# Performance work log

Measured on AMD Instinct MI355X. Metric: run time of the kernel, lower is better.

Reference implementation:

```python
import jax, jax.numpy as jnp
import numpy as np

N = 1048576
INPUT_CH = 3
INPUT_CH_VIEWS = 3
HIDDEN = 64
GEO_FEAT = 15


def setup_inputs() -> dict:
    key = jax.random.key(0)
    ks = jax.random.split(key, 8)
    def w(k, out_d, in_d):
        # torch nn.Linear default init: U(-1/sqrt(in), 1/sqrt(in)), weight shape [out, in]
        bound = 1.0 / np.sqrt(in_d)
        return jax.random.uniform(k, (out_d, in_d), jnp.float32, -bound, bound)
    return {
        "x": jax.random.normal(ks[0], (N, INPUT_CH + INPUT_CH_VIEWS), jnp.float32),
        "sw0": w(ks[1], HIDDEN, INPUT_CH),
        "sw1": w(ks[2], HIDDEN, HIDDEN),
        "sw2": w(ks[3], 1 + GEO_FEAT, HIDDEN),
        "cw0": w(ks[4], HIDDEN, INPUT_CH_VIEWS + GEO_FEAT),
        "cw1": w(ks[5], HIDDEN, HIDDEN),
        "cw2": w(ks[6], HIDDEN, HIDDEN),
        "cw3": w(ks[7], 3, HIDDEN),
    }


def reference(x, sw0, sw1, sw2, cw0, cw1, cw2, cw3):
    input_pts = x[..., :INPUT_CH]          # [N, 3]
    input_views = x[..., INPUT_CH:]        # [N, 3]

    # sigma network: Linear(no bias) + ReLU (no ReLU on last layer)
    h = jax.nn.relu(input_pts @ sw0.T)     # [N, 64]
    h = jax.nn.relu(h @ sw1.T)             # [N, 64]
    h = h @ sw2.T                          # [N, 16]
    sigma = h[..., 0]                      # [N]
    geo_feat = h[..., 1:]                  # [N, 15]

    # color network
    h = jnp.concatenate([input_views, geo_feat], axis=-1)  # [N, 18]
    h = jax.nn.relu(h @ cw0.T)             # [N, 64]
    h = jax.nn.relu(h @ cw1.T)             # [N, 64]
    h = jax.nn.relu(h @ cw2.T)             # [N, 64]
    color = h @ cw3.T                      # [N, 3]

    return jnp.concatenate([color, sigma[..., None]], axis=-1)  # [N, 4]
```

## Files before the change

### kernel.cpp

```cpp
#include <hip/hip_runtime.h>
#include <stdint.h>

typedef __attribute__((ext_vector_type(8))) _Float16 half8;
typedef __attribute__((ext_vector_type(2))) __fp16 fp16x2;
typedef __attribute__((ext_vector_type(16))) float floatx16;
typedef __attribute__((ext_vector_type(2))) short s16x2;
typedef unsigned int u32;
typedef unsigned short u16;


__device__ __forceinline__ u32 pkf16(float a, float b) {
  union { fp16x2 v; u32 u; } c;
  c.v = __builtin_amdgcn_cvt_pkrtz(a, b);
  return c.u;
}

__device__ __forceinline__ u32 relu_pk(u32 t) {
  union { u32 u; s16x2 v; } c;
  c.u = t;
  s16x2 zz = {0, 0};
  c.v = __builtin_elementwise_max(c.v, zz);
  return c.u;
}

__device__ __forceinline__ u16 rtnh(float a) {
  union { _Float16 h; u16 u; } c;
  c.h = (_Float16)a;
  return c.u;
}

__device__ __forceinline__ int sigperm(int k) {
  int r = k & 15;
  int s = (r & 3) | ((r & 4) << 1) | ((r & 8) >> 1);
  return (k & ~15) | s;
}

__device__ __forceinline__ half8 packhalf(const floatx16 a, int base, bool relu) {
  union { u32 u[4]; half8 v; } r;
#pragma unroll
  for (int i = 0; i < 4; ++i) {
    u32 t = pkf16(a[base + 2 * i], a[base + 2 * i + 1]);
    r.u[i] = relu ? relu_pk(t) : t;
  }
  return r.v;
}

#define MFMA(A, B, C) __builtin_amdgcn_mfma_f32_32x32x16_f16(A, B, C, 0, 0, 0)

#define NFRAG 38

__global__ void build_pool(
    const float* __restrict__ w_s0, const float* __restrict__ w_s1,
    const float* __restrict__ w_s2, const float* __restrict__ w_c0,
    const float* __restrict__ w_c1, const float* __restrict__ w_c2,
    const float* __restrict__ w_c3, uint4* __restrict__ pool) {
  const int f = blockIdx.x;
  const int lane = threadIdx.x;
  const int m = lane & 31;
  const int kb = (lane >> 5) << 3;

  union { u16 e[8]; uint4 q; } u;
  if (f < 2) {
    const int row = f * 32 + m;
#pragma unroll
    for (int j = 0; j < 8; ++j) {
      const int k = kb + j;
      u.e[j] = (k < 3) ? rtnh(w_s0[row * 3 + k]) : (u16)0;
    }
  } else if (f < 10) {
    const int g = f - 2, rt = g >> 2, ks = g & 3;
    const int row = rt * 32 + m;
#pragma unroll
    for (int j = 0; j < 8; ++j)
      u.e[j] = rtnh(w_s1[row * 64 + sigperm(ks * 16 + kb + j)]);
  } else if (f < 14) {
    const int ks = f - 10;
    const int row = (m < 16) ? m : 0;
#pragma unroll
    for (int j = 0; j < 8; ++j) {
      u16 v = rtnh(w_s2[row * 64 + sigperm(ks * 16 + kb + j)]);
      u.e[j] = (m < 16) ? v : (u16)0;
    }
  } else if (f < 18) {
    const int g = f - 14, rt = g >> 1, ks = g & 1;
    const int row = rt * 32 + m;
#pragma unroll
    for (int j = 0; j < 8; ++j) {
      if (ks == 0) {
        const int c = sigperm(kb + j);
        u16 v = rtnh(w_c0[row * 18 + (c + 2)]);
        u.e[j] = (c == 0) ? (u16)0 : v;
      } else {
        const int kk = kb + j;
        u16 v = rtnh(w_c0[row * 18 + kk]);
        u.e[j] = (kk < 3) ? v : (u16)0;
      }
    }
  } else if (f < 26) {
    const int g = f - 18, rt = g >> 2, ks = g & 3;
    const int row = rt * 32 + m;
#pragma unroll
    for (int j = 0; j < 8; ++j)
      u.e[j] = rtnh(w_c1[row * 64 + sigperm(ks * 16 + kb + j)]);
  } else if (f < 34) {
    const int g = f - 26, rt = g >> 2, ks = g & 3;
    const int row = rt * 32 + m;
#pragma unroll
    for (int j = 0; j < 8; ++j)
      u.e[j] = rtnh(w_c2[row * 64 + sigperm(ks * 16 + kb + j)]);
  } else {
    const int ks = f - 34;
    const int row = (m < 3) ? m : 0;
#pragma unroll
    for (int j = 0; j < 8; ++j) {
      u16 v = rtnh(w_c3[row * 64 + sigperm(ks * 16 + kb + j)]);
      u.e[j] = (m < 3) ? v : (u16)0;
    }
  }
  pool[f * 64 + lane] = u.q;
}

__global__ __launch_bounds__(256, 2) void nerf_fused(
    const float* __restrict__ x, const uint4* __restrict__ pool,
    float* __restrict__ out, int npts) {
  __shared__ __align__(16) u16 wl[NFRAG * 512];

  {
    uint4* lp = (uint4*)wl;
    for (int i = threadIdx.x; i < NFRAG * 64; i += 256) lp[i] = pool[i];
  }
  __syncthreads();

  const int lane = threadIdx.x & 63;
  const int wid = threadIdx.x >> 6;
  const int m = lane & 31;
  const int hi = lane >> 5;

#define LD(F) (*(const half8*)(wl + (F) * 512 + lane * 8))
#define U4 _Pragma("unroll") for (int s = 0; s < 4; ++s)

  const int ntiles = npts >> 5;
  const int wgid = blockIdx.x * 4 + wid;
  const int tile0 = wgid * 4;
  if (tile0 + 4 > ntiles) return;

  const floatx16 z = (floatx16)0.0f;

  union bfrag { u32 u[4]; half8 v; };
  bfrag bx[4], bv[4];
  int pt[4];
  U4 {
    pt[s] = ((tile0 + s) << 5) | m;
    const float2* xp = (const float2*)(x + (size_t)pt[s] * 6);
    const float2 a0 = xp[0], a1 = xp[1], a2 = xp[2];
    bx[s].u[0] = hi ? 0u : pkf16(a0.x, a0.y);
    bx[s].u[1] = hi ? 0u : pkf16(a1.x, 0.0f);
    bx[s].u[2] = 0u; bx[s].u[3] = 0u;
    bv[s].u[0] = hi ? 0u : pkf16(a1.y, a2.x);
    bv[s].u[1] = hi ? 0u : pkf16(a2.y, 0.0f);
    bv[s].u[2] = 0u; bv[s].u[3] = 0u;
  }

  floatx16 h0[4], h1[4];
  half8 b0[4], b1[4], b2[4], b3[4];
  half8 w;

  w = LD(0); U4 h0[s] = MFMA(w, bx[s].v, z);
  w = LD(1); U4 h1[s] = MFMA(w, bx[s].v, z);
  U4 { b0[s] = packhalf(h0[s], 0, true); b1[s] = packhalf(h0[s], 8, true);
       b2[s] = packhalf(h1[s], 0, true); b3[s] = packhalf(h1[s], 8, true); }

  w = LD(2); U4 h0[s] = MFMA(w, b0[s], z);
  w = LD(6); U4 h1[s] = MFMA(w, b0[s], z);
  w = LD(3); U4 h0[s] = MFMA(w, b1[s], h0[s]);
  w = LD(7); U4 h1[s] = MFMA(w, b1[s], h1[s]);
  w = LD(4); U4 h0[s] = MFMA(w, b2[s], h0[s]);
  w = LD(8); U4 h1[s] = MFMA(w, b2[s], h1[s]);
  w = LD(5); U4 h0[s] = MFMA(w, b3[s], h0[s]);
  w = LD(9); U4 h1[s] = MFMA(w, b3[s], h1[s]);
  U4 { b0[s] = packhalf(h0[s], 0, true); b1[s] = packhalf(h0[s], 8, true);
       b2[s] = packhalf(h1[s], 0, true); b3[s] = packhalf(h1[s], 8, true); }

  w = LD(10); U4 h0[s] = MFMA(w, b0[s], z);
  w = LD(11); U4 h0[s] = MFMA(w, b1[s], h0[s]);
  w = LD(12); U4 h0[s] = MFMA(w, b2[s], h0[s]);
  w = LD(13); U4 h0[s] = MFMA(w, b3[s], h0[s]);
  float sigma[4];
  half8 bs2[4];
  U4 { sigma[s] = h0[s][0]; bs2[s] = packhalf(h0[s], 0, false); }

  w = LD(14); U4 h0[s] = MFMA(w, bs2[s], z);
  w = LD(16); U4 h1[s] = MFMA(w, bs2[s], z);
  w = LD(15); U4 h0[s] = MFMA(w, bv[s].v, h0[s]);
  w = LD(17); U4 h1[s] = MFMA(w, bv[s].v, h1[s]);
  U4 { b0[s] = packhalf(h0[s], 0, true); b1[s] = packhalf(h0[s], 8, true);
       b2[s] = packhalf(h1[s], 0, true); b3[s] = packhalf(h1[s], 8, true); }

  w = LD(18); U4 h0[s] = MFMA(w, b0[s], z);
  w = LD(22); U4 h1[s] = MFMA(w, b0[s], z);
  w = LD(19); U4 h0[s] = MFMA(w, b1[s], h0[s]);
  w = LD(23); U4 h1[s] = MFMA(w, b1[s], h1[s]);
  w = LD(20); U4 h0[s] = MFMA(w, b2[s], h0[s]);
  w = LD(24); U4 h1[s] = MFMA(w, b2[s], h1[s]);
  w = LD(21); U4 h0[s] = MFMA(w, b3[s], h0[s]);
  w = LD(25); U4 h1[s] = MFMA(w, b3[s], h1[s]);
  U4 { b0[s] = packhalf(h0[s], 0, true); b1[s] = packhalf(h0[s], 8, true);
       b2[s] = packhalf(h1[s], 0, true); b3[s] = packhalf(h1[s], 8, true); }

  w = LD(26); U4 h0[s] = MFMA(w, b0[s], z);
  w = LD(30); U4 h1[s] = MFMA(w, b0[s], z);
  w = LD(27); U4 h0[s] = MFMA(w, b1[s], h0[s]);
  w = LD(31); U4 h1[s] = MFMA(w, b1[s], h1[s]);
  w = LD(28); U4 h0[s] = MFMA(w, b2[s], h0[s]);
  w = LD(32); U4 h1[s] = MFMA(w, b2[s], h1[s]);
  w = LD(29); U4 h0[s] = MFMA(w, b3[s], h0[s]);
  w = LD(33); U4 h1[s] = MFMA(w, b3[s], h1[s]);
  U4 { b0[s] = packhalf(h0[s], 0, true); b1[s] = packhalf(h0[s], 8, true);
       b2[s] = packhalf(h1[s], 0, true); b3[s] = packhalf(h1[s], 8, true); }

  w = LD(34); U4 h0[s] = MFMA(w, b0[s], z);
  w = LD(35); U4 h0[s] = MFMA(w, b1[s], h0[s]);
  w = LD(36); U4 h0[s] = MFMA(w, b2[s], h0[s]);
  w = LD(37); U4 h0[s] = MFMA(w, b3[s], h0[s]);

  if (lane < 32) {
    U4 {
      float4 o;
      o.x = h0[s][0]; o.y = h0[s][1]; o.z = h0[s][2]; o.w = sigma[s];
      *(float4*)(out + (size_t)pt[s] * 4) = o;
    }
  }
#undef LD
#undef U4
}

extern "C" void kernel_launch(void* const* d_in, const int* in_sizes, int n_in,
                              void* d_out, int out_size, void* d_ws, size_t ws_size,
                              hipStream_t stream) {
  const float* x = (const float*)d_in[0];
  const float* sw0 = (const float*)d_in[1];
  const float* sw1 = (const float*)d_in[2];
  const float* sw2 = (const float*)d_in[3];
  const float* cw0 = (const float*)d_in[4];
  const float* cw1 = (const float*)d_in[5];
  const float* cw2 = (const float*)d_in[6];
  const float* cw3 = (const float*)d_in[7];
  float* out = (float*)d_out;
  uint4* pool = (uint4*)d_ws;

  const int npts = in_sizes[0] / 6;
  const int ntiles = npts >> 5;
  const int blocks = (ntiles + 15) / 16;

  build_pool<<<NFRAG, 64, 0, stream>>>(sw0, sw1, sw2, cw0, cw1, cw2, cw3, pool);
  nerf_fused<<<blocks, 256, 0, stream>>>(x, pool, out, npts);
}
```

Measured before the change: 115.3 us.

## Keep weight fragments in registers and loop over tiles per wave

Removes the shared-memory weight staging and barrier. Each wave now loads 34 weight fragments straight from global memory into registers and keeps them for a serial loop over 8 tiles, with the last-layer fragments reloaded every iteration. The grid shrinks to match. This cuts LDS traffic and the per-block pool copy, but each tile now runs a single dependent MFMA chain instead of 4 interleaved ones, so latency hiding and register pressure (about 136 VGPRs of weights) may get worse.

```diff
diff --git a/kernel.cpp b/kernel.cpp
--- a/kernel.cpp
+++ b/kernel.cpp
@@ -7,6 +7,8 @@
 typedef __attribute__((ext_vector_type(2))) short s16x2;
 typedef unsigned int u32;
 typedef unsigned short u16;
+
+#define TPW 8
 
 
 __device__ __forceinline__ u32 pkf16(float a, float b) {
@@ -123,115 +125,99 @@
 __global__ __launch_bounds__(256, 2) void nerf_fused(
     const float* __restrict__ x, const uint4* __restrict__ pool,
     float* __restrict__ out, int npts) {
-  __shared__ __align__(16) u16 wl[NFRAG * 512];
-
-  {
-    uint4* lp = (uint4*)wl;
-    for (int i = threadIdx.x; i < NFRAG * 64; i += 256) lp[i] = pool[i];
-  }
-  __syncthreads();
-
   const int lane = threadIdx.x & 63;
   const int wid = threadIdx.x >> 6;
   const int m = lane & 31;
   const int hi = lane >> 5;
 
-#define LD(F) (*(const half8*)(wl + (F) * 512 + lane * 8))
-#define U4 _Pragma("unroll") for (int s = 0; s < 4; ++s)
+#define GW(F) (*(const half8*)((const u16*)pool + (F) * 512 + lane * 8))
+
+  const half8 W0 = GW(0),   W1 = GW(1);
+  const half8 W2 = GW(2),   W3 = GW(3),   W4 = GW(4),   W5 = GW(5);
+  const half8 W6 = GW(6),   W7 = GW(7),   W8 = GW(8),   W9 = GW(9);
+  const half8 W10 = GW(10), W11 = GW(11), W12 = GW(12), W13 = GW(13);
+  const half8 W14 = GW(14), W15 = GW(15), W16 = GW(16), W17 = GW(17);
+  const half8 W18 = GW(18), W19 = GW(19), W20 = GW(20), W21 = GW(21);
+  const half8 W22 = GW(22), W23 = GW(23), W24 = GW(24), W25 = GW(25);
+  const half8 W26 = GW(26), W27 = GW(27), W28 = GW(28), W29 = GW(29);
+  const half8 W30 = GW(30), W31 = GW(31), W32 = GW(32), W33 = GW(33);
 
   const int ntiles = npts >> 5;
-  const int wgid = blockIdx.x * 4 + wid;
-  const int tile0 = wgid * 4;
-  if (tile0 + 4 > ntiles) return;
-
+  const int wave = blockIdx.x * 4 + wid;
   const floatx16 z = (floatx16)0.0f;
 
-  union bfrag { u32 u[4]; half8 v; };
-  bfrag bx[4], bv[4];
-  int pt[4];
-  U4 {
-    pt[s] = ((tile0 + s) << 5) | m;
-    const float2* xp = (const float2*)(x + (size_t)pt[s] * 6);
+#pragma unroll 1
+  for (int t = 0; t < TPW; ++t) {
+    const int tile = wave * TPW + t;
+    if (tile >= ntiles) break;
+    const int pt = (tile << 5) | m;
+
+    const float2* xp = (const float2*)(x + (size_t)pt * 6);
     const float2 a0 = xp[0], a1 = xp[1], a2 = xp[2];
-    bx[s].u[0] = hi ? 0u : pkf16(a0.x, a0.y);
-    bx[s].u[1] = hi ? 0u : pkf16(a1.x, 0.0f);
-    bx[s].u[2] = 0u; bx[s].u[3] = 0u;
-    bv[s].u[0] = hi ? 0u : pkf16(a1.y, a2.x);
-    bv[s].u[1] = hi ? 0u : pkf16(a2.y, 0.0f);
-    bv[s].u[2] = 0u; bv[s].u[3] = 0u;
+
+    union { u32 u[4]; half8 v; } bx, bv;
+    bx.u[0] = hi ? 0u : pkf16(a0.x, a0.y);
+    bx.u[1] = hi ? 0u : pkf16(a1.x, 0.0f);
+    bx.u[2] = 0u; bx.u[3] = 0u;
+    bv.u[0] = hi ? 0u : pkf16(a1.y, a2.x);
+    bv.u[1] = hi ? 0u : pkf16(a2.y, 0.0f);
+    bv.u[2] = 0u; bv.u[3] = 0u;
+
+    floatx16 h0, h1;
+    half8 p0, p1, p2, p3, q0, q1, q2, q3;
+
+    h0 = MFMA(W0, bx.v, z);
+    h1 = MFMA(W1, bx.v, z);
+    p0 = packhalf(h0, 0, true); p1 = packhalf(h0, 8, true);
+    p2 = packhalf(h1, 0, true); p3 = packhalf(h1, 8, true);
+
+    h0 = MFMA(W2, p0, z);  h1 = MFMA(W6, p0, z);
+    h0 = MFMA(W3, p1, h0); h1 = MFMA(W7, p1, h1);
+    h0 = MFMA(W4, p2, h0); h1 = MFMA(W8, p2, h1);
+    h0 = MFMA(W5, p3, h0); h1 = MFMA(W9, p3, h1);
+    q0 = packhalf(h0, 0, true); q1 = packhalf(h0, 8, true);
+    q2 = packhalf(h1, 0, true); q3 = packhalf(h1, 8, true);
+
+    h0 = MFMA(W10, q0, z);
+    h0 = MFMA(W11, q1, h0);
+    h0 = MFMA(W12, q2, h0);
+    h0 = MFMA(W13, q3, h0);
+    const float sigma = h0[0];
+    const half8 bs2 = packhalf(h0, 0, false);
+
+    h0 = MFMA(W14, bs2, z);   h1 = MFMA(W16, bs2, z);
+    h0 = MFMA(W15, bv.v, h0); h1 = MFMA(W17, bv.v, h1);
+    p0 = packhalf(h0, 0, true); p1 = packhalf(h0, 8, true);
+    p2 = packhalf(h1, 0, true); p3 = packhalf(h1, 8, true);
+
+    const half8 C0 = GW(34), C1 = GW(35), C2 = GW(36), C3 = GW(37);
+
+    h0 = MFMA(W18, p0, z);  h1 = MFMA(W22, p0, z);
+    h0 = MFMA(W19, p1, h0); h1 = MFMA(W23, p1, h1);
+    h0 = MFMA(W20, p2, h0); h1 = MFMA(W24, p2, h1);
+    h0 = MFMA(W21, p3, h0); h1 = MFMA(W25, p3, h1);
+    q0 = packhalf(h0, 0, true); q1 = packhalf(h0, 8, true);
+    q2 = packhalf(h1, 0, true); q3 = packhalf(h1, 8, true);
+
+    h0 = MFMA(W26, q0, z);  h1 = MFMA(W30, q0, z);
+    h0 = MFMA(W27, q1, h0); h1 = MFMA(W31, q1, h1);
+    h0 = MFMA(W28, q2, h0); h1 = MFMA(W32, q2, h1);
+    h0 = MFMA(W29, q3, h0); h1 = MFMA(W33, q3, h1);
+    p0 = packhalf(h0, 0, true); p1 = packhalf(h0, 8, true);
+    p2 = packhalf(h1, 0, true); p3 = packhalf(h1, 8, true);
+
+    h0 = MFMA(C0, p0, z);
+    h0 = MFMA(C1, p1, h0);
+    h0 = MFMA(C2, p2, h0);
+    h0 = MFMA(C3, p3, h0);
+
+    if (lane < 32) {
+      float4 o;
+      o.x = h0[0]; o.y = h0[1]; o.z = h0[2]; o.w = sigma;
+      *(float4*)(out + (size_t)pt * 4) = o;
+    }
   }
-
-  floatx16 h0[4], h1[4];
-  half8 b0[4], b1[4], b2[4], b3[4];
-  half8 w;
-
-  w = LD(0); U4 h0[s] = MFMA(w, bx[s].v, z);
-  w = LD(1); U4 h1[s] = MFMA(w, bx[s].v, z);
-  U4 { b0[s] = packhalf(h0[s], 0, true); b1[s] = packhalf(h0[s], 8, true);
-       b2[s] = packhalf(h1[s], 0, true); b3[s] = packhalf(h1[s], 8, true); }
-
-  w = LD(2); U4 h0[s] = MFMA(w, b0[s], z);
-  w = LD(6); U4 h1[s] = MFMA(w, b0[s], z);
-  w = LD(3); U4 h0[s] = MFMA(w, b1[s], h0[s]);
-  w = LD(7); U4 h1[s] = MFMA(w, b1[s], h1[s]);
-  w = LD(4); U4 h0[s] = MFMA(w, b2[s], h0[s]);
-  w = LD(8); U4 h1[s] = MFMA(w, b2[s], h1[s]);
-  w = LD(5); U4 h0[s] = MFMA(w, b3[s], h0[s]);
-  w = LD(9); U4 h1[s] = MFMA(w, b3[s], h1[s]);
-  U4 { b0[s] = packhalf(h0[s], 0, true); b1[s] = packhalf(h0[s], 8, true);
-       b2[s] = packhalf(h1[s], 0, true); b3[s] = packhalf(h1[s], 8, true); }
-
-  w = LD(10); U4 h0[s] = MFMA(w, b0[s], z);
-  w = LD(11); U4 h0[s] = MFMA(w, b1[s], h0[s]);
-  w = LD(12); U4 h0[s] = MFMA(w, b2[s], h0[s]);
-  w = LD(13); U4 h0[s] = MFMA(w, b3[s], h0[s]);
-  float sigma[4];
-  half8 bs2[4];
-  U4 { sigma[s] = h0[s][0]; bs2[s] = packhalf(h0[s], 0, false); }
-
-  w = LD(14); U4 h0[s] = MFMA(w, bs2[s], z);
-  w = LD(16); U4 h1[s] = MFMA(w, bs2[s], z);
-  w = LD(15); U4 h0[s] = MFMA(w, bv[s].v, h0[s]);
-  w = LD(17); U4 h1[s] = MFMA(w, bv[s].v, h1[s]);
-  U4 { b0[s] = packhalf(h0[s], 0, true); b1[s] = packhalf(h0[s], 8, true);
-       b2[s] = packhalf(h1[s], 0, true); b3[s] = packhalf(h1[s], 8, true); }
-
-  w = LD(18); U4 h0[s] = MFMA(w, b0[s], z);
-  w = LD(22); U4 h1[s] = MFMA(w, b0[s], z);
-  w = LD(19); U4 h0[s] = MFMA(w, b1[s], h0[s]);
-  w = LD(23); U4 h1[s] = MFMA(w, b1[s], h1[s]);
-  w = LD(20); U4 h0[s] = MFMA(w, b2[s], h0[s]);
-  w = LD(24); U4 h1[s] = MFMA(w, b2[s], h1[s]);
-  w = LD(21); U4 h0[s] = MFMA(w, b3[s], h0[s]);
-  w = LD(25); U4 h1[s] = MFMA(w, b3[s], h1[s]);
-  U4 { b0[s] = packhalf(h0[s], 0, true); b1[s] = packhalf(h0[s], 8, true);
-       b2[s] = packhalf(h1[s], 0, true); b3[s] = packhalf(h1[s], 8, true); }
-
-  w = LD(26); U4 h0[s] = MFMA(w, b0[s], z);
-  w = LD(30); U4 h1[s] = MFMA(w, b0[s], z);
-  w = LD(27); U4 h0[s] = MFMA(w, b1[s], h0[s]);
-  w = LD(31); U4 h1[s] = MFMA(w, b1[s], h1[s]);
-  w = LD(28); U4 h0[s] = MFMA(w, b2[s], h0[s]);
-  w = LD(32); U4 h1[s] = MFMA(w, b2[s], h1[s]);
-  w = LD(29); U4 h0[s] = MFMA(w, b3[s], h0[s]);
-  w = LD(33); U4 h1[s] = MFMA(w, b3[s], h1[s]);
-  U4 { b0[s] = packhalf(h0[s], 0, true); b1[s] = packhalf(h0[s], 8, true);
-       b2[s] = packhalf(h1[s], 0, true); b3[s] = packhalf(h1[s], 8, true); }
-
-  w = LD(34); U4 h0[s] = MFMA(w, b0[s], z);
-  w = LD(35); U4 h0[s] = MFMA(w, b1[s], h0[s]);
-  w = LD(36); U4 h0[s] = MFMA(w, b2[s], h0[s]);
-  w = LD(37); U4 h0[s] = MFMA(w, b3[s], h0[s]);
-
-  if (lane < 32) {
-    U4 {
-      float4 o;
-      o.x = h0[s][0]; o.y = h0[s][1]; o.z = h0[s][2]; o.w = sigma[s];
-      *(float4*)(out + (size_t)pt[s] * 4) = o;
-    }
-  }
-#undef LD
-#undef U4
+#undef GW
 }
 
 extern "C" void kernel_launch(void* const* d_in, const int* in_sizes, int n_in,
@@ -250,7 +236,7 @@
 
   const int npts = in_sizes[0] / 6;
   const int ntiles = npts >> 5;
-  const int blocks = (ntiles + 15) / 16;
+  const int blocks = (ntiles + 4 * TPW - 1) / (4 * TPW);
 
   build_pool<<<NFRAG, 64, 0, stream>>>(sw0, sw1, sw2, cw0, cw1, cw2, cw3, pool);
   nerf_fused<<<blocks, 256, 0, stream>>>(x, pool, out, npts);
```

Measured after the change: 115.1 us. Within noise of the previous version (-0.2%).
